# Performance work log

Measured on AMD Instinct MI355X. Metric: run time of the kernel, lower is better.

## Reference

```python
import jax, jax.numpy as jnp
import numpy as np

D = 64          # link_state_dim
RU = 256        # readout_units
T = 8           # message-passing iterations
G = 1024        # number of graphs (max graph id + 1)
E = 131072      # number of links (nodes of the line graph)
M = 1048576     # number of edge pairs


def setup_inputs() -> dict:
    key = jax.random.key(0)
    ks = jax.random.split(key, 16)
    s = 0.05
    inp = {
        "states_action": jax.random.normal(ks[0], (E, D), jnp.float32),
        "states_graph_ids": jnp.sort(jax.random.randint(ks[1], (E,), 0, G, jnp.int32)),
        "states_first": jax.random.randint(ks[2], (M,), 0, E, jnp.int32),
        "states_second": jax.random.randint(ks[3], (M,), 0, E, jnp.int32),
        "sates_num_edges": E,
        # Message MLP: Dense(2D -> D), selu
        "W_msg": jax.random.normal(ks[4], (2 * D, D), jnp.float32) * s,
        "b_msg": jnp.zeros((D,), jnp.float32),
        # GRUCell (Keras defaults: reset_after=True)
        "gru_kernel": jax.random.normal(ks[5], (D, 3 * D), jnp.float32) * s,
        "gru_rkernel": jax.random.normal(ks[6], (D, 3 * D), jnp.float32) * s,
        "gru_bias_in": jnp.zeros((3 * D,), jnp.float32),
        "gru_bias_rec": jnp.zeros((3 * D,), jnp.float32),
        # Readout MLP (dropout inactive at inference)
        "W1": jax.random.normal(ks[7], (D, RU), jnp.float32) * s,
        "b1": jnp.zeros((RU,), jnp.float32),
        "W2": jax.random.normal(ks[8], (RU, RU), jnp.float32) * s,
        "b2": jnp.zeros((RU,), jnp.float32),
        "W3": jax.random.normal(ks[9], (RU, 1), jnp.float32) * s,
        "b3": jnp.zeros((1,), jnp.float32),
    }
    return inp


def _gru_cell(x, h, k, rk, bi, br):
    # Keras GRUCell with reset_after=True
    mx = x @ k + bi            # [N, 3D]
    mh = h @ rk + br           # [N, 3D]
    xz, xr, xh = jnp.split(mx, 3, axis=1)
    hz, hr, hh = jnp.split(mh, 3, axis=1)
    z = jax.nn.sigmoid(xz + hz)
    r = jax.nn.sigmoid(xr + hr)
    c = jnp.tanh(xh + r * hh)
    return z * h + (1.0 - z) * c


def reference(states_action, states_graph_ids, states_first, states_second,
              sates_num_edges, W_msg, b_msg, gru_kernel, gru_rkernel,
              gru_bias_in, gru_bias_rec, W1, b1, W2, b2, W3, b3):
    h = states_action                                        # [E, D]
    for _ in range(T):
        pair = jnp.concatenate([h[states_first], h[states_second]], axis=1)  # [M, 2D]
        msg = jax.nn.selu(pair @ W_msg + b_msg)              # [M, D]
        agg = jax.ops.segment_sum(msg, states_second, num_segments=sates_num_edges)  # [E, D]
        h = _gru_cell(agg, h, gru_kernel, gru_rkernel, gru_bias_in, gru_bias_rec)
    g = jax.ops.segment_sum(h, states_graph_ids, num_segments=G)  # [G, D]
    r = jax.nn.selu(g @ W1 + b1)
    r = jax.nn.selu(r @ W2 + b2)
    return r @ W3 + b3                                       # [G, 1]
```

## Files before the change

kernel.cpp:

```cpp
#include <hip/hip_runtime.h>
#include <hip/hip_bf16.h>

#define E_LINKS 131072
#define M_PAIRS 1048576
#define DDIM    64
#define GG      1024
#define RUNITS  256
#define TITER   8

typedef __attribute__((ext_vector_type(8))) short bf16x8;
typedef __attribute__((ext_vector_type(4))) float f32x4;
typedef __attribute__((ext_vector_type(16))) float f32x16;

__device__ inline unsigned short f2bf(float f){
  union { float f; unsigned int u; } v; v.f = f;
  unsigned int u = v.u;
  unsigned int r = (u + 0x7FFFu + ((u >> 16) & 1u)) >> 16;
  return (unsigned short)r;
}
__device__ inline float bf2f(unsigned short u){
  union { unsigned int u; float f; } v; v.u = ((unsigned int)u) << 16; return v.f;
}
__device__ inline float selu_f(float x){
  return x > 0.f ? 1.0507009873554805f * x
                 : 1.7580993408473766f * (__expf(x) - 1.f);
}
__device__ inline float sigmoid_f(float x){ return 1.f / (1.f + __expf(-x)); }
__device__ inline float tanh_f(float x){
  float xc = fminf(fmaxf(x, -15.f), 15.f);
  float e2 = __expf(2.f * xc);
  return (e2 - 1.f) / (e2 + 1.f);
}

__device__ inline bf16x8 packbf8f(float4 u0, float4 u1){
  bf16x8 r;
  r[0] = (short)f2bf(u0.x); r[1] = (short)f2bf(u0.y);
  r[2] = (short)f2bf(u0.z); r[3] = (short)f2bf(u0.w);
  r[4] = (short)f2bf(u1.x); r[5] = (short)f2bf(u1.y);
  r[6] = (short)f2bf(u1.z); r[7] = (short)f2bf(u1.w);
  return r;
}

__device__ inline f32x16 zero16(){
  f32x16 v;
  #pragma unroll
  for (int i = 0; i < 16; i++) v[i] = 0.f;
  return v;
}


__global__ void k_zero(int* __restrict__ counts){
  int i = blockIdx.x * blockDim.x + threadIdx.x;
  if (i < E_LINKS) counts[i] = 0;
}

__global__ void k_hist(const int* __restrict__ second, int* __restrict__ counts){
  int i = blockIdx.x * blockDim.x + threadIdx.x;
  if (i < M_PAIRS) atomicAdd(&counts[second[i]], 1);
}

__global__ __launch_bounds__(256) void k_scan_reduce(const int* __restrict__ counts,
    int* __restrict__ partials){
  __shared__ int s[256];
  int t = threadIdx.x;
  int i = blockIdx.x * 256 + t;
  s[t] = counts[i];
  __syncthreads();
  #pragma unroll
  for (int off = 128; off > 0; off >>= 1){
    if (t < off) s[t] += s[t + off];
    __syncthreads();
  }
  if (t == 0) partials[blockIdx.x] = s[0];
}

__global__ __launch_bounds__(512) void k_scan_part(int* __restrict__ partials){
  __shared__ int s[512];
  int t = threadIdx.x;
  int v = partials[t];
  s[t] = v;
  __syncthreads();
  for (int off = 1; off < 512; off <<= 1){
    int u = (t >= off) ? s[t - off] : 0;
    __syncthreads();
    s[t] += u;
    __syncthreads();
  }
  partials[t] = s[t] - v;
}

__global__ __launch_bounds__(256) void k_scan_apply(const int* __restrict__ counts,
    const int* __restrict__ partials, int* __restrict__ offsets,
    int* __restrict__ cursor){
  __shared__ int s[256];
  int t = threadIdx.x;
  int i = blockIdx.x * 256 + t;
  int c = counts[i];
  s[t] = c;
  __syncthreads();
  for (int off = 1; off < 256; off <<= 1){
    int u = (t >= off) ? s[t - off] : 0;
    __syncthreads();
    s[t] += u;
    __syncthreads();
  }
  int run = partials[blockIdx.x] + s[t] - c;
  offsets[i] = run;
  cursor[i] = run;
  if (i == E_LINKS - 1) offsets[E_LINKS] = run + c;
}

__global__ void k_goffs(const int* __restrict__ gid, int* __restrict__ goffs){
  int i = blockIdx.x * blockDim.x + threadIdx.x;
  if (i >= E_LINKS) return;
  int g = gid[i];
  int gp = (i == 0) ? -1 : gid[i - 1];
  for (int x = gp + 1; x <= g; x++) goffs[x] = i;
  if (i == E_LINKS - 1){
    for (int x = g + 1; x <= GG; x++) goffs[x] = E_LINKS;
  }
}

__global__ void k_scatter(const int* __restrict__ first, const int* __restrict__ second,
    int* __restrict__ cursor, int* __restrict__ srcs){
  int i = blockIdx.x * blockDim.x + threadIdx.x;
  if (i < M_PAIRS){
    int e = second[i];
    int slot = atomicAdd(&cursor[e], 1);
    srcs[slot] = first[i];
  }
}

__global__ void k_prepw(const float* __restrict__ W_msg,
    const float* __restrict__ gk, const float* __restrict__ grk,
    const float* __restrict__ bi, const float* __restrict__ br,
    unsigned short* __restrict__ WzrT, unsigned short* __restrict__ WxhT,
    unsigned short* __restrict__ WhhT, unsigned short* __restrict__ WcT,
    float* __restrict__ bzr, float* __restrict__ bxh, float* __restrict__ bhh){
  int i = blockIdx.x * blockDim.x + threadIdx.x;
  if (i < 16384){
    int c = i >> 7, k = i & 127;
    float v = (k < 64) ? gk[k * 192 + c] : grk[(k - 64) * 192 + c];
    WzrT[i] = f2bf(v);
  } else if (i < 20480){
    int j = i - 16384; int c = j >> 6, k = j & 63;
    WxhT[j] = f2bf(gk[k * 192 + 128 + c]);
  } else if (i < 24576){
    int j = i - 20480; int c = j >> 6, k = j & 63;
    WhhT[j] = f2bf(grk[k * 192 + 128 + c]);
  } else if (i < 32768){
    int j = i - 24576; int c = j >> 6, k = j & 63;
    float v = (c < 64) ? W_msg[k * 64 + c] : W_msg[(64 + k) * 64 + (c - 64)];
    WcT[j] = f2bf(v);
  } else if (i < 33024){
    int j = i - 32768;
    if (j < 128) bzr[j] = bi[j] + br[j];
    else if (j < 192) bxh[j - 128] = bi[j];
    else bhh[j - 192] = br[j - 64];
  }
}


__global__ __launch_bounds__(256) void k_ab0(const float* __restrict__ hf,
    const unsigned short* __restrict__ WcT, const float* __restrict__ b_msg,
    unsigned short* __restrict__ AB){
  int wave = threadIdx.x >> 6, lane = threadIdx.x & 63;
  int row0 = (blockIdx.x * 4 + wave) * 16;
  int lr = lane & 15, lg = lane >> 4;
  f32x4 acc[8];
  #pragma unroll
  for (int i = 0; i < 8; i++) acc[i] = (f32x4){0.f, 0.f, 0.f, 0.f};
  #pragma unroll
  for (int s = 0; s < 2; s++){
    int kb = s * 32 + lg * 8;
    const float* p = hf + (size_t)(row0 + lr) * 64 + kb;
    bf16x8 a = packbf8f(*(const float4*)p, *(const float4*)(p + 4));
    #pragma unroll
    for (int ct = 0; ct < 8; ct++){
      bf16x8 b = *(const bf16x8*)(WcT + (ct * 16 + lr) * 64 + kb);
      acc[ct] = __builtin_amdgcn_mfma_f32_16x16x32_bf16(a, b, acc[ct], 0, 0, 0);
    }
  }
  #pragma unroll
  for (int ct = 0; ct < 8; ct++){
    int col = ct * 16 + lr;
    float bias = (col >= 64) ? b_msg[col - 64] : 0.f;
    #pragma unroll
    for (int q = 0; q < 4; q++){
      int row = row0 + lg * 4 + q;
      AB[(size_t)row * 128 + col] = f2bf(acc[ct][q] + bias);
    }
  }
}

__global__ __launch_bounds__(256) void k_agg(const unsigned short* __restrict__ AB,
    const int* __restrict__ offsets, const int* __restrict__ srcs,
    unsigned short* __restrict__ agg){
  int wave = threadIdx.x >> 6, lane = threadIdx.x & 63;
  int e = blockIdx.x * 4 + wave;
  int g = lane >> 4, d = lane & 15;

  ushort4 bq = *(const ushort4*)(AB + (size_t)e * 128 + 64 + d * 4);
  float b0 = bf2f(bq.x), b1 = bf2f(bq.y), b2 = bf2f(bq.z), b3 = bf2f(bq.w);

  int beg = offsets[e], end = offsets[e + 1];
  float a0 = 0.f, a1 = 0.f, a2 = 0.f, a3 = 0.f;

  int i = beg + g;
  for (; i + 4 < end; i += 8){
    int s0 = srcs[i];
    int s1 = srcs[i + 4];
    ushort4 q0 = *(const ushort4*)(AB + (size_t)s0 * 128 + d * 4);
    ushort4 q1 = *(const ushort4*)(AB + (size_t)s1 * 128 + d * 4);
    a0 += selu_f(bf2f(q0.x) + b0);
    a1 += selu_f(bf2f(q0.y) + b1);
    a2 += selu_f(bf2f(q0.z) + b2);
    a3 += selu_f(bf2f(q0.w) + b3);
    a0 += selu_f(bf2f(q1.x) + b0);
    a1 += selu_f(bf2f(q1.y) + b1);
    a2 += selu_f(bf2f(q1.z) + b2);
    a3 += selu_f(bf2f(q1.w) + b3);
  }
  if (i < end){
    int s0 = srcs[i];
    ushort4 q0 = *(const ushort4*)(AB + (size_t)s0 * 128 + d * 4);
    a0 += selu_f(bf2f(q0.x) + b0);
    a1 += selu_f(bf2f(q0.y) + b1);
    a2 += selu_f(bf2f(q0.z) + b2);
    a3 += selu_f(bf2f(q0.w) + b3);
  }

  a0 += __shfl_xor(a0, 16, 64); a0 += __shfl_xor(a0, 32, 64);
  a1 += __shfl_xor(a1, 16, 64); a1 += __shfl_xor(a1, 32, 64);
  a2 += __shfl_xor(a2, 16, 64); a2 += __shfl_xor(a2, 32, 64);
  a3 += __shfl_xor(a3, 16, 64); a3 += __shfl_xor(a3, 32, 64);

  if (g == 0){
    ushort4 o;
    o.x = f2bf(a0); o.y = f2bf(a1); o.z = f2bf(a2); o.w = f2bf(a3);
    *(ushort4*)(agg + (size_t)e * 64 + d * 4) = o;
  }
}

template<bool WITH_AB>
__global__ __launch_bounds__(256, 4) void k_fused(const unsigned short* __restrict__ agg,
    const float* h_in, float* h_out,
    const unsigned short* __restrict__ WzrT, const unsigned short* __restrict__ WxhT,
    const unsigned short* __restrict__ WhhT, const unsigned short* __restrict__ WcT,
    const float* __restrict__ bzr, const float* __restrict__ bxh,
    const float* __restrict__ bhh,
    const float* __restrict__ b_msg, unsigned short* __restrict__ AB){
  __shared__ float hsh[4][32][68];
  int wave = threadIdx.x >> 6, lane = threadIdx.x & 63;
  int row0 = (blockIdx.x * 4 + wave) * 32;
  int lc = lane & 31, lh = lane >> 5;
  unsigned short* tsh = (unsigned short*)&hsh[wave][0][0];

  bf16x8 az[8];
  const unsigned short* arow = agg + (size_t)(row0 + lc) * 64 + lh * 8;
  #pragma unroll
  for (int s = 0; s < 4; s++) az[s] = *(const bf16x8*)(arow + s * 16);
  const float* hrow = h_in + (size_t)(row0 + lc) * 64 + lh * 8;
  #pragma unroll
  for (int s = 0; s < 4; s++){
    float4 u0 = *(const float4*)(hrow + s * 16);
    float4 u1 = *(const float4*)(hrow + s * 16 + 4);
    az[4 + s] = packbf8f(u0, u1);
    *(float4*)(&hsh[wave][lc][s * 16 + lh * 8]) = u0;
    *(float4*)(&hsh[wave][lc][s * 16 + lh * 8 + 4]) = u1;
  }

  f32x16 ar0 = zero16(), ar1 = zero16();
  #pragma unroll
  for (int s = 0; s < 8; s++){
    const unsigned short* wk = WzrT + lh * 8 + s * 16;
    bf16x8 b2 = *(const bf16x8*)(wk + (size_t)(64 + lc) * 128);
    bf16x8 b3 = *(const bf16x8*)(wk + (size_t)(96 + lc) * 128);
    ar0 = __builtin_amdgcn_mfma_f32_32x32x16_bf16(az[s], b2, ar0, 0, 0, 0);
    ar1 = __builtin_amdgcn_mfma_f32_32x32x16_bf16(az[s], b3, ar1, 0, 0, 0);
  }

  float cv[2][16];

  {
    f32x16 axh = zero16(), ahh = zero16();
    #pragma unroll
    for (int s = 0; s < 4; s++){
      const unsigned short* wx = WxhT + lh * 8 + s * 16;
      axh = __builtin_amdgcn_mfma_f32_32x32x16_bf16(az[s],
          *(const bf16x8*)(wx + (size_t)lc * 64), axh, 0, 0, 0);
      const unsigned short* wh = WhhT + lh * 8 + s * 16;
      ahh = __builtin_amdgcn_mfma_f32_32x32x16_bf16(az[4 + s],
          *(const bf16x8*)(wh + (size_t)lc * 64), ahh, 0, 0, 0);
    }
    float brv = bzr[64 + lc], bx = bxh[lc], bh = bhh[lc];
    #pragma unroll
    for (int r = 0; r < 16; r++){
      float rr = sigmoid_f(ar0[r] + brv);
      cv[0][r] = tanh_f(axh[r] + bx + rr * (ahh[r] + bh));
    }
  }

  {
    f32x16 axh = zero16(), ahh = zero16();
    #pragma unroll
    for (int s = 0; s < 4; s++){
      const unsigned short* wx = WxhT + lh * 8 + s * 16;
      axh = __builtin_amdgcn_mfma_f32_32x32x16_bf16(az[s],
          *(const bf16x8*)(wx + (size_t)(32 + lc) * 64), axh, 0, 0, 0);
      const unsigned short* wh = WhhT + lh * 8 + s * 16;
      ahh = __builtin_amdgcn_mfma_f32_32x32x16_bf16(az[4 + s],
          *(const bf16x8*)(wh + (size_t)(32 + lc) * 64), ahh, 0, 0, 0);
    }
    float brv = bzr[64 + 32 + lc], bx = bxh[32 + lc], bh = bhh[32 + lc];
    #pragma unroll
    for (int r = 0; r < 16; r++){
      float rr = sigmoid_f(ar1[r] + brv);
      cv[1][r] = tanh_f(axh[r] + bx + rr * (ahh[r] + bh));
    }
  }

  f32x16 azt0 = zero16(), azt1 = zero16();
  #pragma unroll
  for (int s = 0; s < 8; s++){
    const unsigned short* wk = WzrT + lh * 8 + s * 16;
    bf16x8 b0 = *(const bf16x8*)(wk + (size_t)lc * 128);
    bf16x8 b1 = *(const bf16x8*)(wk + (size_t)(32 + lc) * 128);
    azt0 = __builtin_amdgcn_mfma_f32_32x32x16_bf16(az[s], b0, azt0, 0, 0, 0);
    azt1 = __builtin_amdgcn_mfma_f32_32x32x16_bf16(az[s], b1, azt1, 0, 0, 0);
  }

  {
    float bz0 = bzr[lc], bz1 = bzr[32 + lc];
    #pragma unroll
    for (int r = 0; r < 16; r++){
      int rl = (r & 3) + 8 * (r >> 2) + 4 * lh;
      float h0 = hsh[wave][rl][lc];
      float h1 = hsh[wave][rl][32 + lc];
      float z0 = sigmoid_f(azt0[r] + bz0);
      float z1 = sigmoid_f(azt1[r] + bz1);
      cv[0][r] = z0 * h0 + (1.f - z0) * cv[0][r];
      cv[1][r] = z1 * h1 + (1.f - z1) * cv[1][r];
    }
  }

  __syncthreads();

  {
    int j0 = lc, j1 = 32 + lc;
    #pragma unroll
    for (int r = 0; r < 16; r++){
      int rl = (r & 3) + 8 * (r >> 2) + 4 * lh;
      size_t base = (size_t)(row0 + rl) * 64;
      h_out[base + j0] = cv[0][r];
      h_out[base + j1] = cv[1][r];
      if (WITH_AB){
        tsh[rl * 64 + (((j0 >> 3) ^ (rl & 7)) << 3) + (j0 & 7)] = f2bf(cv[0][r]);
        tsh[rl * 64 + (((j1 >> 3) ^ (rl & 7)) << 3) + (j1 & 7)] = f2bf(cv[1][r]);
      }
    }
  }

  if (WITH_AB){
    f32x16 acc[4];
    #pragma unroll
    for (int i = 0; i < 4; i++) acc[i] = zero16();
    #pragma unroll
    for (int s = 0; s < 4; s++){
      int blk = ((s * 2 + lh) ^ (lc & 7)) << 3;
      bf16x8 a = *(const bf16x8*)(&tsh[lc * 64 + blk]);
      const unsigned short* wc = WcT + lh * 8 + s * 16;
      #pragma unroll
      for (int ct = 0; ct < 4; ct++){
        bf16x8 b = *(const bf16x8*)(wc + (size_t)(ct * 32 + lc) * 64);
        acc[ct] = __builtin_amdgcn_mfma_f32_32x32x16_bf16(a, b, acc[ct], 0, 0, 0);
      }
    }
    #pragma unroll
    for (int ct = 0; ct < 4; ct++){
      int col = ct * 32 + lc;
      float bias = (col >= 64) ? b_msg[col - 64] : 0.f;
      #pragma unroll
      for (int r = 0; r < 16; r++){
        int rl = (r & 3) + 8 * (r >> 2) + 4 * lh;
        AB[(size_t)(row0 + rl) * 128 + col] = f2bf(acc[ct][r] + bias);
      }
    }
  }
}


__global__ __launch_bounds__(256) void k_seg(const float* __restrict__ hf,
    const int* __restrict__ goff, float* __restrict__ gsum){
  int wave = threadIdx.x >> 6, lane = threadIdx.x & 63;
  int g = blockIdx.x * 4 + wave;
  int beg = goff[g], end = goff[g + 1];
  float acc = 0.f;
  for (int e = beg; e < end; e++) acc += hf[(size_t)e * 64 + lane];
  gsum[(size_t)g * 64 + lane] = acc;
}

__global__ __launch_bounds__(256) void k_mlp(const float* __restrict__ gsum,
    const float* __restrict__ W1, const float* __restrict__ b1,
    const float* __restrict__ W2, const float* __restrict__ b2,
    const float* __restrict__ W3, const float* __restrict__ b3,
    float* __restrict__ out){
  __shared__ float sg[64];
  __shared__ float sr1[256];
  __shared__ float sr2[256];
  __shared__ float wsum[4];
  int g = blockIdx.x, t = threadIdx.x;
  if (t < 64) sg[t] = gsum[(size_t)g * 64 + t];
  __syncthreads();
  float a = b1[t];
  #pragma unroll
  for (int k = 0; k < 64; k++) a += sg[k] * W1[k * 256 + t];
  sr1[t] = selu_f(a);
  __syncthreads();
  float b = b2[t];
  for (int k = 0; k < 256; k++) b += sr1[k] * W2[k * 256 + t];
  sr2[t] = selu_f(b);
  __syncthreads();
  float v = sr2[t] * W3[t];
  for (int off = 32; off > 0; off >>= 1) v += __shfl_down(v, off, 64);
  if ((t & 63) == 0) wsum[t >> 6] = v;
  __syncthreads();
  if (t == 0) out[g] = wsum[0] + wsum[1] + wsum[2] + wsum[3] + b3[0];
}


static inline size_t alignup(size_t x){ return (x + 255) & ~(size_t)255; }

extern "C" void kernel_launch(void* const* d_in, const int* in_sizes, int n_in,
                              void* d_out, int out_size, void* d_ws, size_t ws_size,
                              hipStream_t stream) {
  const float* states_action = (const float*)d_in[0];
  const int*   graph_ids     = (const int*)d_in[1];
  const int*   first         = (const int*)d_in[2];
  const int*   second        = (const int*)d_in[3];
  const float* W_msg         = (const float*)d_in[5];
  const float* b_msg         = (const float*)d_in[6];
  const float* gk            = (const float*)d_in[7];
  const float* grk           = (const float*)d_in[8];
  const float* bi            = (const float*)d_in[9];
  const float* br            = (const float*)d_in[10];
  const float* W1            = (const float*)d_in[11];
  const float* b1            = (const float*)d_in[12];
  const float* W2            = (const float*)d_in[13];
  const float* b2            = (const float*)d_in[14];
  const float* W3            = (const float*)d_in[15];
  const float* b3            = (const float*)d_in[16];
  float* out = (float*)d_out;

  char* ws = (char*)d_ws;
  size_t off = 0;
  float*          h_f32  = (float*)(ws + off);          off += alignup((size_t)E_LINKS * 64 * 4);
  unsigned short* aggb   = (unsigned short*)(ws + off); off += alignup((size_t)E_LINKS * 64 * 2);
  unsigned short* AB     = (unsigned short*)(ws + off); off += alignup((size_t)E_LINKS * 128 * 2);
  unsigned short* WzrT   = (unsigned short*)(ws + off); off += alignup(128 * 128 * 2);
  unsigned short* WxhT   = (unsigned short*)(ws + off); off += alignup(64 * 64 * 2);
  unsigned short* WhhT   = (unsigned short*)(ws + off); off += alignup(64 * 64 * 2);
  unsigned short* WcT    = (unsigned short*)(ws + off); off += alignup(128 * 64 * 2);
  float*          bzr    = (float*)(ws + off);          off += alignup(128 * 4);
  float*          bxhv   = (float*)(ws + off);          off += alignup(64 * 4);
  float*          bhhv   = (float*)(ws + off);          off += alignup(64 * 4);
  int*            counts = (int*)(ws + off);            off += alignup((size_t)E_LINKS * 4);
  int*            offs   = (int*)(ws + off);            off += alignup(((size_t)E_LINKS + 1) * 4);
  int*            cursor = (int*)(ws + off);            off += alignup((size_t)E_LINKS * 4);
  int*            srcs   = (int*)(ws + off);            off += alignup((size_t)M_PAIRS * 4);
  int*            parts  = (int*)(ws + off);            off += alignup(512 * 4);
  int*            goffs  = (int*)(ws + off);            off += alignup(((size_t)GG + 1) * 4);
  float*          gsum   = (float*)(ws + off);          off += alignup((size_t)GG * 64 * 4);

  dim3 b256(256);

  k_zero<<<dim3(E_LINKS / 256), b256, 0, stream>>>(counts);
  k_hist<<<dim3(M_PAIRS / 256), b256, 0, stream>>>(second, counts);
  k_scan_reduce<<<dim3(512), b256, 0, stream>>>(counts, parts);
  k_scan_part<<<dim3(1), dim3(512), 0, stream>>>(parts);
  k_scan_apply<<<dim3(512), b256, 0, stream>>>(counts, parts, offs, cursor);
  k_goffs<<<dim3(E_LINKS / 256), b256, 0, stream>>>(graph_ids, goffs);
  k_scatter<<<dim3(M_PAIRS / 256), b256, 0, stream>>>(first, second, cursor, srcs);

  k_prepw<<<dim3(129), b256, 0, stream>>>(W_msg, gk, grk, bi, br,
      WzrT, WxhT, WhhT, WcT, bzr, bxhv, bhhv);

  k_ab0<<<dim3(E_LINKS / 64), b256, 0, stream>>>(states_action, WcT, b_msg, AB);

  for (int t = 0; t < TITER; t++){
    k_agg<<<dim3(E_LINKS / 4), b256, 0, stream>>>(AB, offs, srcs, aggb);
    const float* h_in = (t == 0) ? states_action : h_f32;
    if (t < TITER - 1)
      k_fused<true><<<dim3(E_LINKS / 128), b256, 0, stream>>>(aggb, h_in, h_f32,
          WzrT, WxhT, WhhT, WcT, bzr, bxhv, bhhv, b_msg, AB);
    else
      k_fused<false><<<dim3(E_LINKS / 128), b256, 0, stream>>>(aggb, h_in, h_f32,
          WzrT, WxhT, WhhT, WcT, bzr, bxhv, bhhv, b_msg, AB);
  }

  k_seg<<<dim3(GG / 4), b256, 0, stream>>>(h_f32, goffs, gsum);
  k_mlp<<<dim3(GG), b256, 0, stream>>>(gsum, W1, b1, W2, b2, W3, b3, out);
}
```

Baseline: 989.7 us.

## Fuse edge aggregation into GRU kernel with ping-pong AB buffers

Folds the separate gather/segment-sum kernel into the fused GRU kernel. Each wave now aggregates its own 32 rows into swizzled shared memory instead of writing and re-reading an agg buffer in global memory. The AB projection buffer is double-buffered because other blocks still read the previous iteration's AB while this one writes the next. This removes a launch and the agg round trip per iteration. The cost is much lower gather parallelism: 1024 blocks with serial per-row loops replace 32K wave-per-row blocks, so latency hiding for random gathers may suffer.

```diff
diff --git a/kernel.cpp b/kernel.cpp
--- a/kernel.cpp
+++ b/kernel.cpp
@@ -193,81 +193,80 @@
   }
 }
 
-__global__ __launch_bounds__(256) void k_agg(const unsigned short* __restrict__ AB,
+template<bool WITH_AB>
+__global__ __launch_bounds__(256, 4) void k_fused(
+    const unsigned short* __restrict__ ABi,
     const int* __restrict__ offsets, const int* __restrict__ srcs,
-    unsigned short* __restrict__ agg){
-  int wave = threadIdx.x >> 6, lane = threadIdx.x & 63;
-  int e = blockIdx.x * 4 + wave;
-  int g = lane >> 4, d = lane & 15;
-
-  ushort4 bq = *(const ushort4*)(AB + (size_t)e * 128 + 64 + d * 4);
-  float b0 = bf2f(bq.x), b1 = bf2f(bq.y), b2 = bf2f(bq.z), b3 = bf2f(bq.w);
-
-  int beg = offsets[e], end = offsets[e + 1];
-  float a0 = 0.f, a1 = 0.f, a2 = 0.f, a3 = 0.f;
-
-  int i = beg + g;
-  for (; i + 4 < end; i += 8){
-    int s0 = srcs[i];
-    int s1 = srcs[i + 4];
-    ushort4 q0 = *(const ushort4*)(AB + (size_t)s0 * 128 + d * 4);
-    ushort4 q1 = *(const ushort4*)(AB + (size_t)s1 * 128 + d * 4);
-    a0 += selu_f(bf2f(q0.x) + b0);
-    a1 += selu_f(bf2f(q0.y) + b1);
-    a2 += selu_f(bf2f(q0.z) + b2);
-    a3 += selu_f(bf2f(q0.w) + b3);
-    a0 += selu_f(bf2f(q1.x) + b0);
-    a1 += selu_f(bf2f(q1.y) + b1);
-    a2 += selu_f(bf2f(q1.z) + b2);
-    a3 += selu_f(bf2f(q1.w) + b3);
-  }
-  if (i < end){
-    int s0 = srcs[i];
-    ushort4 q0 = *(const ushort4*)(AB + (size_t)s0 * 128 + d * 4);
-    a0 += selu_f(bf2f(q0.x) + b0);
-    a1 += selu_f(bf2f(q0.y) + b1);
-    a2 += selu_f(bf2f(q0.z) + b2);
-    a3 += selu_f(bf2f(q0.w) + b3);
-  }
-
-  a0 += __shfl_xor(a0, 16, 64); a0 += __shfl_xor(a0, 32, 64);
-  a1 += __shfl_xor(a1, 16, 64); a1 += __shfl_xor(a1, 32, 64);
-  a2 += __shfl_xor(a2, 16, 64); a2 += __shfl_xor(a2, 32, 64);
-  a3 += __shfl_xor(a3, 16, 64); a3 += __shfl_xor(a3, 32, 64);
-
-  if (g == 0){
-    ushort4 o;
-    o.x = f2bf(a0); o.y = f2bf(a1); o.z = f2bf(a2); o.w = f2bf(a3);
-    *(ushort4*)(agg + (size_t)e * 64 + d * 4) = o;
-  }
-}
-
-template<bool WITH_AB>
-__global__ __launch_bounds__(256, 4) void k_fused(const unsigned short* __restrict__ agg,
     const float* h_in, float* h_out,
     const unsigned short* __restrict__ WzrT, const unsigned short* __restrict__ WxhT,
     const unsigned short* __restrict__ WhhT, const unsigned short* __restrict__ WcT,
     const float* __restrict__ bzr, const float* __restrict__ bxh,
     const float* __restrict__ bhh,
-    const float* __restrict__ b_msg, unsigned short* __restrict__ AB){
+    const float* __restrict__ b_msg, unsigned short* __restrict__ ABo){
   __shared__ float hsh[4][32][68];
   int wave = threadIdx.x >> 6, lane = threadIdx.x & 63;
   int row0 = (blockIdx.x * 4 + wave) * 32;
   int lc = lane & 31, lh = lane >> 5;
-  unsigned short* tsh = (unsigned short*)&hsh[wave][0][0];
+  unsigned short* ash = (unsigned short*)&hsh[wave][0][0];
+
+  const float* hrow = h_in + (size_t)(row0 + lc) * 64 + lh * 8;
+  float4 hu0[4], hu1[4];
+  #pragma unroll
+  for (int s = 0; s < 4; s++){
+    hu0[s] = *(const float4*)(hrow + s * 16);
+    hu1[s] = *(const float4*)(hrow + s * 16 + 4);
+  }
+
+  {
+    int g = lane >> 4, d = lane & 15;
+    #pragma unroll 1
+    for (int eo = 0; eo < 8; eo++){
+      int r = g * 8 + eo;
+      int e = row0 + r;
+      ushort4 bq = *(const ushort4*)(ABi + (size_t)e * 128 + 64 + d * 4);
+      float b0 = bf2f(bq.x), b1 = bf2f(bq.y), b2 = bf2f(bq.z), b3 = bf2f(bq.w);
+      int beg = offsets[e], end = offsets[e + 1];
+      float a0 = 0.f, a1 = 0.f, a2 = 0.f, a3 = 0.f;
+      int i = beg;
+      for (; i + 1 < end; i += 2){
+        int s0 = srcs[i], s1 = srcs[i + 1];
+        ushort4 q0 = *(const ushort4*)(ABi + (size_t)s0 * 128 + d * 4);
+        ushort4 q1 = *(const ushort4*)(ABi + (size_t)s1 * 128 + d * 4);
+        a0 += selu_f(bf2f(q0.x) + b0);
+        a1 += selu_f(bf2f(q0.y) + b1);
+        a2 += selu_f(bf2f(q0.z) + b2);
+        a3 += selu_f(bf2f(q0.w) + b3);
+        a0 += selu_f(bf2f(q1.x) + b0);
+        a1 += selu_f(bf2f(q1.y) + b1);
+        a2 += selu_f(bf2f(q1.z) + b2);
+        a3 += selu_f(bf2f(q1.w) + b3);
+      }
+      if (i < end){
+        int s0 = srcs[i];
+        ushort4 q0 = *(const ushort4*)(ABi + (size_t)s0 * 128 + d * 4);
+        a0 += selu_f(bf2f(q0.x) + b0);
+        a1 += selu_f(bf2f(q0.y) + b1);
+        a2 += selu_f(bf2f(q0.z) + b2);
+        a3 += selu_f(bf2f(q0.w) + b3);
+      }
+      ushort4 o;
+      o.x = f2bf(a0); o.y = f2bf(a1); o.z = f2bf(a2); o.w = f2bf(a3);
+      *(ushort4*)(ash + r * 64 + (((d >> 1) ^ (r & 7)) << 3) + (d & 1) * 4) = o;
+    }
+  }
 
   bf16x8 az[8];
-  const unsigned short* arow = agg + (size_t)(row0 + lc) * 64 + lh * 8;
-  #pragma unroll
-  for (int s = 0; s < 4; s++) az[s] = *(const bf16x8*)(arow + s * 16);
-  const float* hrow = h_in + (size_t)(row0 + lc) * 64 + lh * 8;
+  #pragma unroll
+  for (int s = 0; s < 4; s++)
+    az[s] = *(const bf16x8*)(ash + lc * 64 + (((s * 2 + lh) ^ (lc & 7)) << 3));
+
+  __syncthreads();
+
   #pragma unroll
   for (int s = 0; s < 4; s++){
-    float4 u0 = *(const float4*)(hrow + s * 16);
-    float4 u1 = *(const float4*)(hrow + s * 16 + 4);
-    az[4 + s] = packbf8f(u0, u1);
-    *(float4*)(&hsh[wave][lc][s * 16 + lh * 8]) = u0;
-    *(float4*)(&hsh[wave][lc][s * 16 + lh * 8 + 4]) = u1;
+    az[4 + s] = packbf8f(hu0[s], hu1[s]);
+    *(float4*)(&hsh[wave][lc][s * 16 + lh * 8]) = hu0[s];
+    *(float4*)(&hsh[wave][lc][s * 16 + lh * 8 + 4]) = hu1[s];
   }
 
   f32x16 ar0 = zero16(), ar1 = zero16();
@@ -346,6 +345,7 @@
 
   __syncthreads();
 
+  unsigned short* tsh = ash;
   {
     int j0 = lc, j1 = 32 + lc;
     #pragma unroll
@@ -383,7 +383,7 @@
       #pragma unroll
       for (int r = 0; r < 16; r++){
         int rl = (r & 3) + 8 * (r >> 2) + 4 * lh;
-        AB[(size_t)(row0 + rl) * 128 + col] = f2bf(acc[ct][r] + bias);
+        ABo[(size_t)(row0 + rl) * 128 + col] = f2bf(acc[ct][r] + bias);
       }
     }
   }
@@ -455,8 +455,8 @@
   char* ws = (char*)d_ws;
   size_t off = 0;
   float*          h_f32  = (float*)(ws + off);          off += alignup((size_t)E_LINKS * 64 * 4);
-  unsigned short* aggb   = (unsigned short*)(ws + off); off += alignup((size_t)E_LINKS * 64 * 2);
-  unsigned short* AB     = (unsigned short*)(ws + off); off += alignup((size_t)E_LINKS * 128 * 2);
+  unsigned short* AB0    = (unsigned short*)(ws + off); off += alignup((size_t)E_LINKS * 128 * 2);
+  unsigned short* AB1    = (unsigned short*)(ws + off); off += alignup((size_t)E_LINKS * 128 * 2);
   unsigned short* WzrT   = (unsigned short*)(ws + off); off += alignup(128 * 128 * 2);
   unsigned short* WxhT   = (unsigned short*)(ws + off); off += alignup(64 * 64 * 2);
   unsigned short* WhhT   = (unsigned short*)(ws + off); off += alignup(64 * 64 * 2);
@@ -485,17 +485,22 @@
   k_prepw<<<dim3(129), b256, 0, stream>>>(W_msg, gk, grk, bi, br,
       WzrT, WxhT, WhhT, WcT, bzr, bxhv, bhhv);
 
-  k_ab0<<<dim3(E_LINKS / 64), b256, 0, stream>>>(states_action, WcT, b_msg, AB);
-
+  k_ab0<<<dim3(E_LINKS / 64), b256, 0, stream>>>(states_action, WcT, b_msg, AB0);
+
+  const unsigned short* abin = AB0;
+  unsigned short* about = AB1;
   for (int t = 0; t < TITER; t++){
-    k_agg<<<dim3(E_LINKS / 4), b256, 0, stream>>>(AB, offs, srcs, aggb);
     const float* h_in = (t == 0) ? states_action : h_f32;
-    if (t < TITER - 1)
-      k_fused<true><<<dim3(E_LINKS / 128), b256, 0, stream>>>(aggb, h_in, h_f32,
-          WzrT, WxhT, WhhT, WcT, bzr, bxhv, bhhv, b_msg, AB);
-    else
-      k_fused<false><<<dim3(E_LINKS / 128), b256, 0, stream>>>(aggb, h_in, h_f32,
-          WzrT, WxhT, WhhT, WcT, bzr, bxhv, bhhv, b_msg, AB);
+    if (t < TITER - 1){
+      k_fused<true><<<dim3(E_LINKS / 128), b256, 0, stream>>>(abin, offs, srcs,
+          h_in, h_f32, WzrT, WxhT, WhhT, WcT, bzr, bxhv, bhhv, b_msg, about);
+      const unsigned short* tmp = abin;
+      abin = about;
+      about = (unsigned short*)tmp;
+    } else {
+      k_fused<false><<<dim3(E_LINKS / 128), b256, 0, stream>>>(abin, offs, srcs,
+          h_in, h_f32, WzrT, WxhT, WhhT, WcT, bzr, bxhv, bhhv, b_msg, about);
+    }
   }
 
   k_seg<<<dim3(GG / 4), b256, 0, stream>>>(h_f32, goffs, gsum);
```

Result: slower. 1.043 ms (+5.4%).

## Split GRU fused kernel columns across two waves per 32-row tile

Applied to the files above, without the earlier changes.

Each 32-row tile of the GRU/AB fused kernel is now handled by two waves, each computing half of the output columns, using 512-thread blocks. The h tile is staged cooperatively in shared memory behind an extra barrier, and both waves read it back to build the bf16 operand. This halves the per-wave accumulators and MFMA chains to raise occupancy and latency hiding. The cost is duplicated agg loads and operand packing in both waves, plus extra block-wide syncs.

```diff
diff --git a/kernel.cpp b/kernel.cpp
--- a/kernel.cpp
+++ b/kernel.cpp
@@ -243,7 +243,7 @@
 }
 
 template<bool WITH_AB>
-__global__ __launch_bounds__(256, 4) void k_fused(const unsigned short* __restrict__ agg,
+__global__ __launch_bounds__(512, 8) void k_fused(const unsigned short* __restrict__ agg,
     const float* h_in, float* h_out,
     const unsigned short* __restrict__ WzrT, const unsigned short* __restrict__ WxhT,
     const unsigned short* __restrict__ WhhT, const unsigned short* __restrict__ WcT,
@@ -252,133 +252,111 @@
     const float* __restrict__ b_msg, unsigned short* __restrict__ AB){
   __shared__ float hsh[4][32][68];
   int wave = threadIdx.x >> 6, lane = threadIdx.x & 63;
-  int row0 = (blockIdx.x * 4 + wave) * 32;
+  int grp = wave >> 1, sh = wave & 1;
+  int row0 = (blockIdx.x * 4 + grp) * 32;
   int lc = lane & 31, lh = lane >> 5;
-  unsigned short* tsh = (unsigned short*)&hsh[wave][0][0];
+  int J = sh * 32;
+
+  {
+    const float* p = h_in + (size_t)(row0 + lc) * 64 + J + lh * 16;
+    float4 u0 = *(const float4*)(p);
+    float4 u1 = *(const float4*)(p + 4);
+    float4 u2 = *(const float4*)(p + 8);
+    float4 u3 = *(const float4*)(p + 12);
+    float* q = &hsh[grp][lc][J + lh * 16];
+    *(float4*)(q)      = u0;
+    *(float4*)(q + 4)  = u1;
+    *(float4*)(q + 8)  = u2;
+    *(float4*)(q + 12) = u3;
+  }
+  __syncthreads();
 
   bf16x8 az[8];
   const unsigned short* arow = agg + (size_t)(row0 + lc) * 64 + lh * 8;
   #pragma unroll
   for (int s = 0; s < 4; s++) az[s] = *(const bf16x8*)(arow + s * 16);
-  const float* hrow = h_in + (size_t)(row0 + lc) * 64 + lh * 8;
   #pragma unroll
   for (int s = 0; s < 4; s++){
-    float4 u0 = *(const float4*)(hrow + s * 16);
-    float4 u1 = *(const float4*)(hrow + s * 16 + 4);
+    float4 u0 = *(const float4*)(&hsh[grp][lc][s * 16 + lh * 8]);
+    float4 u1 = *(const float4*)(&hsh[grp][lc][s * 16 + lh * 8 + 4]);
     az[4 + s] = packbf8f(u0, u1);
-    *(float4*)(&hsh[wave][lc][s * 16 + lh * 8]) = u0;
-    *(float4*)(&hsh[wave][lc][s * 16 + lh * 8 + 4]) = u1;
-  }
-
-  f32x16 ar0 = zero16(), ar1 = zero16();
+  }
+
+  f32x16 ar = zero16();
   #pragma unroll
   for (int s = 0; s < 8; s++){
-    const unsigned short* wk = WzrT + lh * 8 + s * 16;
-    bf16x8 b2 = *(const bf16x8*)(wk + (size_t)(64 + lc) * 128);
-    bf16x8 b3 = *(const bf16x8*)(wk + (size_t)(96 + lc) * 128);
-    ar0 = __builtin_amdgcn_mfma_f32_32x32x16_bf16(az[s], b2, ar0, 0, 0, 0);
-    ar1 = __builtin_amdgcn_mfma_f32_32x32x16_bf16(az[s], b3, ar1, 0, 0, 0);
-  }
-
-  float cv[2][16];
-
+    bf16x8 b = *(const bf16x8*)(WzrT + (size_t)(64 + J + lc) * 128 + lh * 8 + s * 16);
+    ar = __builtin_amdgcn_mfma_f32_32x32x16_bf16(az[s], b, ar, 0, 0, 0);
+  }
+
+  float cv[16];
   {
     f32x16 axh = zero16(), ahh = zero16();
     #pragma unroll
     for (int s = 0; s < 4; s++){
-      const unsigned short* wx = WxhT + lh * 8 + s * 16;
-      axh = __builtin_amdgcn_mfma_f32_32x32x16_bf16(az[s],
-          *(const bf16x8*)(wx + (size_t)lc * 64), axh, 0, 0, 0);
-      const unsigned short* wh = WhhT + lh * 8 + s * 16;
-      ahh = __builtin_amdgcn_mfma_f32_32x32x16_bf16(az[4 + s],
-          *(const bf16x8*)(wh + (size_t)lc * 64), ahh, 0, 0, 0);
-    }
-    float brv = bzr[64 + lc], bx = bxh[lc], bh = bhh[lc];
+      bf16x8 bx = *(const bf16x8*)(WxhT + (size_t)(J + lc) * 64 + lh * 8 + s * 16);
+      axh = __builtin_amdgcn_mfma_f32_32x32x16_bf16(az[s], bx, axh, 0, 0, 0);
+      bf16x8 bh = *(const bf16x8*)(WhhT + (size_t)(J + lc) * 64 + lh * 8 + s * 16);
+      ahh = __builtin_amdgcn_mfma_f32_32x32x16_bf16(az[4 + s], bh, ahh, 0, 0, 0);
+    }
+    float brv = bzr[64 + J + lc], bx = bxh[J + lc], bh = bhh[J + lc];
     #pragma unroll
     for (int r = 0; r < 16; r++){
-      float rr = sigmoid_f(ar0[r] + brv);
-      cv[0][r] = tanh_f(axh[r] + bx + rr * (ahh[r] + bh));
-    }
+      float rr = sigmoid_f(ar[r] + brv);
+      cv[r] = tanh_f(axh[r] + bx + rr * (ahh[r] + bh));
+    }
+  }
+
+  f32x16 azt = zero16();
+  #pragma unroll
+  for (int s = 0; s < 8; s++){
+    bf16x8 b = *(const bf16x8*)(WzrT + (size_t)(J + lc) * 128 + lh * 8 + s * 16);
+    azt = __builtin_amdgcn_mfma_f32_32x32x16_bf16(az[s], b, azt, 0, 0, 0);
   }
 
   {
-    f32x16 axh = zero16(), ahh = zero16();
-    #pragma unroll
-    for (int s = 0; s < 4; s++){
-      const unsigned short* wx = WxhT + lh * 8 + s * 16;
-      axh = __builtin_amdgcn_mfma_f32_32x32x16_bf16(az[s],
-          *(const bf16x8*)(wx + (size_t)(32 + lc) * 64), axh, 0, 0, 0);
-      const unsigned short* wh = WhhT + lh * 8 + s * 16;
-      ahh = __builtin_amdgcn_mfma_f32_32x32x16_bf16(az[4 + s],
-          *(const bf16x8*)(wh + (size_t)(32 + lc) * 64), ahh, 0, 0, 0);
-    }
-    float brv = bzr[64 + 32 + lc], bx = bxh[32 + lc], bh = bhh[32 + lc];
-    #pragma unroll
-    for (int r = 0; r < 16; r++){
-      float rr = sigmoid_f(ar1[r] + brv);
-      cv[1][r] = tanh_f(axh[r] + bx + rr * (ahh[r] + bh));
-    }
-  }
-
-  f32x16 azt0 = zero16(), azt1 = zero16();
-  #pragma unroll
-  for (int s = 0; s < 8; s++){
-    const unsigned short* wk = WzrT + lh * 8 + s * 16;
-    bf16x8 b0 = *(const bf16x8*)(wk + (size_t)lc * 128);
-    bf16x8 b1 = *(const bf16x8*)(wk + (size_t)(32 + lc) * 128);
-    azt0 = __builtin_amdgcn_mfma_f32_32x32x16_bf16(az[s], b0, azt0, 0, 0, 0);
-    azt1 = __builtin_amdgcn_mfma_f32_32x32x16_bf16(az[s], b1, azt1, 0, 0, 0);
-  }
-
-  {
-    float bz0 = bzr[lc], bz1 = bzr[32 + lc];
+    float bz = bzr[J + lc];
     #pragma unroll
     for (int r = 0; r < 16; r++){
       int rl = (r & 3) + 8 * (r >> 2) + 4 * lh;
-      float h0 = hsh[wave][rl][lc];
-      float h1 = hsh[wave][rl][32 + lc];
-      float z0 = sigmoid_f(azt0[r] + bz0);
-      float z1 = sigmoid_f(azt1[r] + bz1);
-      cv[0][r] = z0 * h0 + (1.f - z0) * cv[0][r];
-      cv[1][r] = z1 * h1 + (1.f - z1) * cv[1][r];
-    }
-  }
-
-  __syncthreads();
-
+      float h0 = hsh[grp][rl][J + lc];
+      float z = sigmoid_f(azt[r] + bz);
+      cv[r] = z * h0 + (1.f - z) * cv[r];
+    }
+  }
+
+  __syncthreads();
+
+  unsigned short* tsh = (unsigned short*)&hsh[grp][0][0];
   {
-    int j0 = lc, j1 = 32 + lc;
+    int j = J + lc;
     #pragma unroll
     for (int r = 0; r < 16; r++){
       int rl = (r & 3) + 8 * (r >> 2) + 4 * lh;
-      size_t base = (size_t)(row0 + rl) * 64;
-      h_out[base + j0] = cv[0][r];
-      h_out[base + j1] = cv[1][r];
-      if (WITH_AB){
-        tsh[rl * 64 + (((j0 >> 3) ^ (rl & 7)) << 3) + (j0 & 7)] = f2bf(cv[0][r]);
-        tsh[rl * 64 + (((j1 >> 3) ^ (rl & 7)) << 3) + (j1 & 7)] = f2bf(cv[1][r]);
-      }
+      h_out[(size_t)(row0 + rl) * 64 + j] = cv[r];
+      if (WITH_AB)
+        tsh[rl * 64 + (((j >> 3) ^ (rl & 7)) << 3) + (j & 7)] = f2bf(cv[r]);
     }
   }
 
   if (WITH_AB){
-    f32x16 acc[4];
-    #pragma unroll
-    for (int i = 0; i < 4; i++) acc[i] = zero16();
+    __syncthreads();
+    f32x16 acc[2];
+    acc[0] = zero16(); acc[1] = zero16();
     #pragma unroll
     for (int s = 0; s < 4; s++){
       int blk = ((s * 2 + lh) ^ (lc & 7)) << 3;
       bf16x8 a = *(const bf16x8*)(&tsh[lc * 64 + blk]);
-      const unsigned short* wc = WcT + lh * 8 + s * 16;
       #pragma unroll
-      for (int ct = 0; ct < 4; ct++){
-        bf16x8 b = *(const bf16x8*)(wc + (size_t)(ct * 32 + lc) * 64);
+      for (int ct = 0; ct < 2; ct++){
+        int col = sh * 64 + ct * 32 + lc;
+        bf16x8 b = *(const bf16x8*)(WcT + (size_t)col * 64 + lh * 8 + s * 16);
         acc[ct] = __builtin_amdgcn_mfma_f32_32x32x16_bf16(a, b, acc[ct], 0, 0, 0);
       }
     }
     #pragma unroll
-    for (int ct = 0; ct < 4; ct++){
-      int col = ct * 32 + lc;
+    for (int ct = 0; ct < 2; ct++){
+      int col = sh * 64 + ct * 32 + lc;
       float bias = (col >= 64) ? b_msg[col - 64] : 0.f;
       #pragma unroll
       for (int r = 0; r < 16; r++){
@@ -491,10 +469,10 @@
     k_agg<<<dim3(E_LINKS / 4), b256, 0, stream>>>(AB, offs, srcs, aggb);
     const float* h_in = (t == 0) ? states_action : h_f32;
     if (t < TITER - 1)
-      k_fused<true><<<dim3(E_LINKS / 128), b256, 0, stream>>>(aggb, h_in, h_f32,
+      k_fused<true><<<dim3(E_LINKS / 128), dim3(512), 0, stream>>>(aggb, h_in, h_f32,
           WzrT, WxhT, WhhT, WcT, bzr, bxhv, bhhv, b_msg, AB);
     else
-      k_fused<false><<<dim3(E_LINKS / 128), b256, 0, stream>>>(aggb, h_in, h_f32,
+      k_fused<false><<<dim3(E_LINKS / 128), dim3(512), 0, stream>>>(aggb, h_in, h_f32,
           WzrT, WxhT, WhhT, WcT, bzr, bxhv, bhhv, b_msg, AB);
   }
 
```

Result: slower. 2.067 ms (+108.9%).
